# Kernel tuning notes

Hardware: AMD Instinct MI355X
Metric: run time of the kernel (lower is better)

Reference implementation:

```python
import jax, jax.numpy as jnp
import numpy as np

DS = 16
NUM_INPUTS = 13
WIDTH = 64
DEPTH = 5
NUM_OUTPUTS = 3
# channels of the per-pixel MLP: input gets 4*log2(ds) cosine coord channels
CH = [NUM_INPUTS + 4 * int(np.log2(DS))] + [WIDTH] * (DEPTH - 1) + [NUM_OUTPUTS]


def _splits():
    biases, weights, idx = [], [], 0
    for l in range(len(CH) - 1):
        nci, nco = CH[l], CH[l + 1]
        biases.append((idx, idx + nco)); idx += nco
        weights.append((idx, idx + nco * nci)); idx += nco * nci
    return biases, weights, idx

BIAS_SPLITS, WEIGHT_SPLITS, NUM_PARAMS = _splits()


def _get_coords(bs, h, w, ds):
    """Cosine positional encoding, 4 channels per octave of ds."""
    two_pi = 2.0 * np.pi
    chans = []
    f = ds
    x = jnp.arange(w, dtype=jnp.float32)
    y = jnp.arange(h, dtype=jnp.float32)
    while f > 1:
        px = two_pi * jnp.remainder(x, f) / f  # [w]
        py = two_pi * jnp.remainder(y, f) / f  # [h]
        xcos = jnp.broadcast_to(jnp.cos(px)[None, None, None, :], (bs, 1, h, w))
        xsin = jnp.broadcast_to(jnp.sin(px)[None, None, None, :], (bs, 1, h, w))
        ycos = jnp.broadcast_to(jnp.cos(py)[None, None, :, None], (bs, 1, h, w))
        ysin = jnp.broadcast_to(jnp.sin(py)[None, None, :, None], (bs, 1, h, w))
        chans += [xcos, xsin, ycos, ysin]
        f //= 2
    return jnp.concatenate(chans, axis=1)  # [bs, 4*log2(ds), h, w]


def setup_inputs() -> dict:
    key = jax.random.key(0)
    k1, k2 = jax.random.split(key)
    bs, h, w = 4, 512, 512
    h_lr, w_lr = h // DS, w // DS
    highres = jax.random.normal(k1, (bs, NUM_INPUTS, h, w), dtype=jnp.float32)
    lr_params = jax.random.normal(k2, (bs, NUM_PARAMS, h_lr, w_lr), dtype=jnp.float32)
    return {"highres": highres, "lr_params": lr_params}


def reference(highres, lr_params):
    k = DS
    bs, _, h, w = highres.shape
    _, _, h_lr, w_lr = lr_params.shape

    coords = _get_coords(bs, h, w, k)
    x = jnp.concatenate([highres, coords], axis=1)  # [bs, nci0, h, w]
    nci0 = x.shape[1]

    # unfold into k*k tiles per low-res pixel: [bs, h_lr, w_lr, k*k, nci0]
    tiles = (x.reshape(bs, nci0, h_lr, k, w_lr, k)
              .transpose(0, 2, 4, 3, 5, 1)
              .reshape(bs, h_lr, w_lr, k * k, nci0))

    out = tiles
    n_layers = len(CH) - 1
    for l in range(n_layers):
        nci, nco = CH[l], CH[l + 1]
        ws, we = WEIGHT_SPLITS[l]
        b0, b1 = BIAS_SPLITS[l]
        w_ = (lr_params[:, ws:we].transpose(0, 2, 3, 1)
              .reshape(bs, h_lr, w_lr, nci, nco))
        b_ = (lr_params[:, b0:b1].transpose(0, 2, 3, 1)
              .reshape(bs, h_lr, w_lr, 1, nco))
        out = jnp.einsum('bhwpi,bhwio->bhwpo', out, w_) + b_
        if l < n_layers - 1:
            out = jnp.where(out >= 0, out, 0.01 * out)  # leaky_relu(0.01)
        else:
            out = jnp.tanh(out)

    # fold tiles back to [bs, num_outputs, h, w]
    out = (out.reshape(bs, h_lr, w_lr, k, k, NUM_OUTPUTS)
            .transpose(0, 5, 1, 3, 2, 4)
            .reshape(bs, NUM_OUTPUTS, h, w))
    return out
```

## Files before the change

### kernel.cpp

```cpp
#include <hip/hip_runtime.h>
#include <math.h>

#define NCH   14595
#define WROW  14596
#define HR_C  13
#define IMG_H 512
#define IMG_W 512
#define BS    4


__global__ __launch_bounds__(256) void transpose_params(const float* __restrict__ lp,
                                                        float* __restrict__ wsT) {
    __shared__ float tile[64][65];
    int bid = blockIdx.x;
    int pt = bid & 15;
    int t  = bid >> 4;
    int ct = t % 229;
    int b  = t / 229;
    int c0 = ct * 64, p0 = pt * 64;
    int tp = threadIdx.x & 63;
    int tr = threadIdx.x >> 6;
#pragma unroll
    for (int s = 0; s < 16; s++) {
        int c = c0 + tr + s * 4;
        if (c < NCH)
            tile[tr + s * 4][tp] = lp[((size_t)b * NCH + c) * 1024 + p0 + tp];
    }
    __syncthreads();
#pragma unroll
    for (int s = 0; s < 16; s++) {
        int p = p0 + tr + s * 4;
        int c = c0 + tp;
        if (c < NCH)
            wsT[((size_t)b * 1024 + p) * WROW + c] = tile[tp][tr + s * 4];
    }
}

__device__ __forceinline__ void block_sync_lds() {
    __builtin_amdgcn_sched_barrier(0);
    asm volatile("s_waitcnt lgkmcnt(0)" ::: "memory");
    __builtin_amdgcn_s_barrier();
    __builtin_amdgcn_sched_barrier(0);
}

template<int NCI>
__device__ __forceinline__ void mlp_layer(const float* __restrict__ actT,
                                          const float* __restrict__ wbuf,
                                          int px0, int o0, float acc[4][8]) {
#pragma unroll
    for (int j = 0; j < 8; j++) {
        float bv = wbuf[o0 + j];
        acc[0][j] = bv; acc[1][j] = bv; acc[2][j] = bv; acc[3][j] = bv;
    }
#pragma unroll 4
    for (int k = 0; k < NCI; k++) {
        float4 a  = *(const float4*)&actT[k * 128 + px0];
        float4 w0 = *(const float4*)&wbuf[64 + (k << 6) + o0];
        float4 w1 = *(const float4*)&wbuf[64 + (k << 6) + o0 + 4];
        float av[4] = {a.x, a.y, a.z, a.w};
        float wv[8] = {w0.x, w0.y, w0.z, w0.w, w1.x, w1.y, w1.z, w1.w};
#pragma unroll
        for (int i = 0; i < 4; i++)
#pragma unroll
            for (int j = 0; j < 8; j++)
                acc[i][j] = fmaf(av[i], wv[j], acc[i][j]);
    }
}

__global__ __launch_bounds__(256, 3) void asap_main(const float* __restrict__ hr,
                                                    const float* __restrict__ lp,
                                                    const float* __restrict__ wsT,
                                                    float* __restrict__ out,
                                                    int use_ws) {
    __shared__ __align__(16) float actT[64 * 128];
    __shared__ __align__(16) float wbuf[4160];

    int bid0 = blockIdx.x;
    int bid  = ((bid0 & 7) << 10) | (bid0 >> 3);

    int half = bid & 1;
    int x    = (bid >> 1) & 31;
    int y    = (bid >> 6) & 31;
    int b    = bid >> 11;
    int tid  = threadIdx.x;
    int pix  = y * 32 + x;

    const size_t wrow_base = ((size_t)b * 1024 + pix) * WROW;
    const float* lp_base   = lp + (size_t)b * NCH * 1024 + pix;

    float4 rv[5];
    float  rt0 = 0.f;
    auto stage_load = [&](int off, int len) {
        int n4 = len >> 2;
        if (use_ws) {
            const float4* s4 = (const float4*)(wsT + wrow_base + off);
#pragma unroll
            for (int i = 0; i < 5; i++) {
                int j = tid + (i << 8);
                if (j < n4) rv[i] = s4[j];
            }
            if (tid < (len & 3)) rt0 = wsT[wrow_base + off + (len & ~3) + tid];
        } else {
#pragma unroll
            for (int i = 0; i < 5; i++) {
                int j = tid + (i << 8);
                if (j < n4) {
                    int e = off + (j << 2);
                    rv[i].x = lp_base[(size_t)(e + 0) << 10];
                    rv[i].y = lp_base[(size_t)(e + 1) << 10];
                    rv[i].z = lp_base[(size_t)(e + 2) << 10];
                    rv[i].w = lp_base[(size_t)(e + 3) << 10];
                }
            }
            if (tid < (len & 3)) rt0 = lp_base[(size_t)(off + (len & ~3) + tid) << 10];
        }
    };
    auto stage_store = [&](int len) {
        int n4 = len >> 2;
        float4* d4 = (float4*)wbuf;
#pragma unroll
        for (int i = 0; i < 5; i++) {
            int j = tid + (i << 8);
            if (j < n4) d4[j] = rv[i];
        }
        if (tid < (len & 3)) wbuf[(len & ~3) + tid] = rt0;
    };

    {
        if (use_ws) {
            const float4* s4 = (const float4*)(wsT + wrow_base);
            float4* d4 = (float4*)wbuf;
            for (int j = tid; j < 480; j += 256) d4[j] = s4[j];
        } else {
            for (int j = tid; j < 1920; j += 256) wbuf[j] = lp_base[(size_t)j << 10];
        }
        int Y0 = y * 16 + half * 8, X0 = x * 16;
        for (int t = tid; t < HR_C * 128; t += 256) {
            int c = t >> 7, p = t & 127;
            int row = p >> 4, kx = p & 15;
            actT[c * 128 + p] =
                hr[(((size_t)b * HR_C + c) * IMG_H + Y0 + row) * IMG_W + X0 + kx];
        }
        if (tid < 128) {
            int p = tid, row = p >> 4, kx = p & 15;
            int kyg = half * 8 + row;
            const float two_pi = 6.28318530717958647692f;
            int f = 16;
#pragma unroll
            for (int fi = 0; fi < 4; fi++) {
                float ax = two_pi * (float)(kx & (f - 1)) / (float)f;
                float ay = two_pi * (float)(kyg & (f - 1)) / (float)f;
                actT[(13 + 4 * fi + 0) * 128 + p] = cosf(ax);
                actT[(13 + 4 * fi + 1) * 128 + p] = sinf(ax);
                actT[(13 + 4 * fi + 2) * 128 + p] = cosf(ay);
                actT[(13 + 4 * fi + 3) * 128 + p] = sinf(ay);
                f >>= 1;
            }
        }
    }
    block_sync_lds();

    int pg = tid & 31, og = tid >> 5;
    int px0 = pg << 2, o0 = og << 3;
    float acc[4][8];

    auto writeback = [&]() {
#pragma unroll
        for (int j = 0; j < 8; j++) {
            float4 v;
            v.x = acc[0][j]; v.y = acc[1][j]; v.z = acc[2][j]; v.w = acc[3][j];
            v.x = v.x >= 0.f ? v.x : 0.01f * v.x;
            v.y = v.y >= 0.f ? v.y : 0.01f * v.y;
            v.z = v.z >= 0.f ? v.z : 0.01f * v.z;
            v.w = v.w >= 0.f ? v.w : 0.01f * v.w;
            *(float4*)&actT[(o0 + j) * 128 + px0] = v;
        }
    };

    stage_load(1920, 4160);
    mlp_layer<29>(actT, wbuf, px0, o0, acc);
    block_sync_lds();
    writeback();
    stage_store(4160);
    block_sync_lds();

    stage_load(6080, 4160);
    mlp_layer<64>(actT, wbuf, px0, o0, acc);
    block_sync_lds();
    writeback();
    stage_store(4160);
    block_sync_lds();

    stage_load(10240, 4160);
    mlp_layer<64>(actT, wbuf, px0, o0, acc);
    block_sync_lds();
    writeback();
    stage_store(4160);
    block_sync_lds();

    stage_load(14400, 195);
    mlp_layer<64>(actT, wbuf, px0, o0, acc);
    block_sync_lds();
    writeback();
    stage_store(195);
    block_sync_lds();

    if (tid < 128) {
        int p = tid;
        float s0 = wbuf[0], s1 = wbuf[1], s2 = wbuf[2];
#pragma unroll 4
        for (int k = 0; k < 64; k++) {
            float a = actT[k * 128 + p];
            s0 = fmaf(a, wbuf[3 + k * 3 + 0], s0);
            s1 = fmaf(a, wbuf[3 + k * 3 + 1], s1);
            s2 = fmaf(a, wbuf[3 + k * 3 + 2], s2);
        }
        int row = p >> 4, kx = p & 15;
        int Y = y * 16 + half * 8 + row, X = x * 16 + kx;
        size_t base = ((size_t)b * 3) * IMG_H * IMG_W + (size_t)Y * IMG_W + X;
        out[base]                             = tanhf(s0);
        out[base + (size_t)IMG_H * IMG_W]     = tanhf(s1);
        out[base + (size_t)2 * IMG_H * IMG_W] = tanhf(s2);
    }
}

extern "C" void kernel_launch(void* const* d_in, const int* in_sizes, int n_in,
                              void* d_out, int out_size, void* d_ws, size_t ws_size,
                              hipStream_t stream) {
    const float* hr = (const float*)d_in[0];
    const float* lp = (const float*)d_in[1];
    float* out = (float*)d_out;
    float* wsT = (float*)d_ws;

    size_t need = (size_t)BS * 1024 * WROW * sizeof(float);
    int use_ws = (ws_size >= need) ? 1 : 0;

    if (use_ws) {
        transpose_params<<<BS * 229 * 16, 256, 0, stream>>>(lp, wsT);
    }
    asap_main<<<8192, 256, 0, stream>>>(hr, lp, wsT, out, use_ws);
}
```

Measured before the change: 533.9 us.

## Read per-pixel weights directly from global memory instead of staging in LDS

Removes the LDS weight buffer and its register-staged prefetch, so each thread reads its weight float4s and biases straight from the transposed workspace row, which goes through the cache since all threads in a block share one row. Freeing LDS lets the launch bound rise to four blocks per SIMD group, and the use_ws branch becomes a template parameter. Leaky-relu becomes fmaxf. The cost is that weight loads now hit global memory or cache latency inside the FMA inner loop instead of LDS, and the overlap of the next layer's weight prefetch with compute is lost.

```diff
diff --git a/kernel.cpp b/kernel.cpp
--- a/kernel.cpp
+++ b/kernel.cpp
@@ -43,37 +43,63 @@
     __builtin_amdgcn_sched_barrier(0);
 }
 
-template<int NCI>
+template<int NCI, bool USE_WS>
 __device__ __forceinline__ void mlp_layer(const float* __restrict__ actT,
-                                          const float* __restrict__ wbuf,
+                                          const float* __restrict__ wrow,
+                                          const float* __restrict__ lp_col,
+                                          int loff,
                                           int px0, int o0, float acc[4][8]) {
-#pragma unroll
-    for (int j = 0; j < 8; j++) {
-        float bv = wbuf[o0 + j];
-        acc[0][j] = bv; acc[1][j] = bv; acc[2][j] = bv; acc[3][j] = bv;
+    if (USE_WS) {
+        float4 b0 = *(const float4*)&wrow[o0];
+        float4 b1 = *(const float4*)&wrow[o0 + 4];
+#pragma unroll
+        for (int i = 0; i < 4; i++) {
+            acc[i][0] = b0.x; acc[i][1] = b0.y; acc[i][2] = b0.z; acc[i][3] = b0.w;
+            acc[i][4] = b1.x; acc[i][5] = b1.y; acc[i][6] = b1.z; acc[i][7] = b1.w;
+        }
+    } else {
+#pragma unroll
+        for (int j = 0; j < 8; j++) {
+            float bv = lp_col[(size_t)(loff + o0 + j) << 10];
+#pragma unroll
+            for (int i = 0; i < 4; i++) acc[i][j] = bv;
+        }
     }
 #pragma unroll 4
     for (int k = 0; k < NCI; k++) {
-        float4 a  = *(const float4*)&actT[k * 128 + px0];
-        float4 w0 = *(const float4*)&wbuf[64 + (k << 6) + o0];
-        float4 w1 = *(const float4*)&wbuf[64 + (k << 6) + o0 + 4];
-        float av[4] = {a.x, a.y, a.z, a.w};
-        float wv[8] = {w0.x, w0.y, w0.z, w0.w, w1.x, w1.y, w1.z, w1.w};
-#pragma unroll
-        for (int i = 0; i < 4; i++)
-#pragma unroll
-            for (int j = 0; j < 8; j++)
-                acc[i][j] = fmaf(av[i], wv[j], acc[i][j]);
-    }
-}
-
-__global__ __launch_bounds__(256, 3) void asap_main(const float* __restrict__ hr,
+        float4 a = *(const float4*)&actT[k * 128 + px0];
+        float4 w0, w1;
+        if (USE_WS) {
+            w0 = *(const float4*)&wrow[64 + (k << 6) + o0];
+            w1 = *(const float4*)&wrow[64 + (k << 6) + o0 + 4];
+        } else {
+            int e = loff + 64 + (k << 6) + o0;
+            w0.x = lp_col[(size_t)(e + 0) << 10]; w0.y = lp_col[(size_t)(e + 1) << 10];
+            w0.z = lp_col[(size_t)(e + 2) << 10]; w0.w = lp_col[(size_t)(e + 3) << 10];
+            w1.x = lp_col[(size_t)(e + 4) << 10]; w1.y = lp_col[(size_t)(e + 5) << 10];
+            w1.z = lp_col[(size_t)(e + 6) << 10]; w1.w = lp_col[(size_t)(e + 7) << 10];
+        }
+#pragma unroll
+        for (int i = 0; i < 4; i++) {
+            float av = (i == 0) ? a.x : (i == 1) ? a.y : (i == 2) ? a.z : a.w;
+            acc[i][0] = fmaf(av, w0.x, acc[i][0]);
+            acc[i][1] = fmaf(av, w0.y, acc[i][1]);
+            acc[i][2] = fmaf(av, w0.z, acc[i][2]);
+            acc[i][3] = fmaf(av, w0.w, acc[i][3]);
+            acc[i][4] = fmaf(av, w1.x, acc[i][4]);
+            acc[i][5] = fmaf(av, w1.y, acc[i][5]);
+            acc[i][6] = fmaf(av, w1.z, acc[i][6]);
+            acc[i][7] = fmaf(av, w1.w, acc[i][7]);
+        }
+    }
+}
+
+template<bool USE_WS>
+__global__ __launch_bounds__(256, 4) void asap_main(const float* __restrict__ hr,
                                                     const float* __restrict__ lp,
                                                     const float* __restrict__ wsT,
-                                                    float* __restrict__ out,
-                                                    int use_ws) {
+                                                    float* __restrict__ out) {
     __shared__ __align__(16) float actT[64 * 128];
-    __shared__ __align__(16) float wbuf[4160];
 
     int bid0 = blockIdx.x;
     int bid  = ((bid0 & 7) << 10) | (bid0 >> 3);
@@ -85,55 +111,10 @@
     int tid  = threadIdx.x;
     int pix  = y * 32 + x;
 
-    const size_t wrow_base = ((size_t)b * 1024 + pix) * WROW;
-    const float* lp_base   = lp + (size_t)b * NCH * 1024 + pix;
-
-    float4 rv[5];
-    float  rt0 = 0.f;
-    auto stage_load = [&](int off, int len) {
-        int n4 = len >> 2;
-        if (use_ws) {
-            const float4* s4 = (const float4*)(wsT + wrow_base + off);
-#pragma unroll
-            for (int i = 0; i < 5; i++) {
-                int j = tid + (i << 8);
-                if (j < n4) rv[i] = s4[j];
-            }
-            if (tid < (len & 3)) rt0 = wsT[wrow_base + off + (len & ~3) + tid];
-        } else {
-#pragma unroll
-            for (int i = 0; i < 5; i++) {
-                int j = tid + (i << 8);
-                if (j < n4) {
-                    int e = off + (j << 2);
-                    rv[i].x = lp_base[(size_t)(e + 0) << 10];
-                    rv[i].y = lp_base[(size_t)(e + 1) << 10];
-                    rv[i].z = lp_base[(size_t)(e + 2) << 10];
-                    rv[i].w = lp_base[(size_t)(e + 3) << 10];
-                }
-            }
-            if (tid < (len & 3)) rt0 = lp_base[(size_t)(off + (len & ~3) + tid) << 10];
-        }
-    };
-    auto stage_store = [&](int len) {
-        int n4 = len >> 2;
-        float4* d4 = (float4*)wbuf;
-#pragma unroll
-        for (int i = 0; i < 5; i++) {
-            int j = tid + (i << 8);
-            if (j < n4) d4[j] = rv[i];
-        }
-        if (tid < (len & 3)) wbuf[(len & ~3) + tid] = rt0;
-    };
+    const float* wrow   = wsT + ((size_t)b * 1024 + pix) * WROW;
+    const float* lp_col = lp + (size_t)b * NCH * 1024 + pix;
 
     {
-        if (use_ws) {
-            const float4* s4 = (const float4*)(wsT + wrow_base);
-            float4* d4 = (float4*)wbuf;
-            for (int j = tid; j < 480; j += 256) d4[j] = s4[j];
-        } else {
-            for (int j = tid; j < 1920; j += 256) wbuf[j] = lp_base[(size_t)j << 10];
-        }
         int Y0 = y * 16 + half * 8, X0 = x * 16;
         for (int t = tid; t < HR_C * 128; t += 256) {
             int c = t >> 7, p = t & 127;
@@ -169,51 +150,60 @@
         for (int j = 0; j < 8; j++) {
             float4 v;
             v.x = acc[0][j]; v.y = acc[1][j]; v.z = acc[2][j]; v.w = acc[3][j];
-            v.x = v.x >= 0.f ? v.x : 0.01f * v.x;
-            v.y = v.y >= 0.f ? v.y : 0.01f * v.y;
-            v.z = v.z >= 0.f ? v.z : 0.01f * v.z;
-            v.w = v.w >= 0.f ? v.w : 0.01f * v.w;
+            v.x = fmaxf(v.x, 0.01f * v.x);
+            v.y = fmaxf(v.y, 0.01f * v.y);
+            v.z = fmaxf(v.z, 0.01f * v.z);
+            v.w = fmaxf(v.w, 0.01f * v.w);
             *(float4*)&actT[(o0 + j) * 128 + px0] = v;
         }
     };
 
-    stage_load(1920, 4160);
-    mlp_layer<29>(actT, wbuf, px0, o0, acc);
-    block_sync_lds();
-    writeback();
-    stage_store(4160);
-    block_sync_lds();
-
-    stage_load(6080, 4160);
-    mlp_layer<64>(actT, wbuf, px0, o0, acc);
-    block_sync_lds();
-    writeback();
-    stage_store(4160);
-    block_sync_lds();
-
-    stage_load(10240, 4160);
-    mlp_layer<64>(actT, wbuf, px0, o0, acc);
-    block_sync_lds();
-    writeback();
-    stage_store(4160);
-    block_sync_lds();
-
-    stage_load(14400, 195);
-    mlp_layer<64>(actT, wbuf, px0, o0, acc);
-    block_sync_lds();
-    writeback();
-    stage_store(195);
+    mlp_layer<29, USE_WS>(actT, wrow + 0,     lp_col, 0,     px0, o0, acc);
+    block_sync_lds();
+    writeback();
+    block_sync_lds();
+
+    mlp_layer<64, USE_WS>(actT, wrow + 1920,  lp_col, 1920,  px0, o0, acc);
+    block_sync_lds();
+    writeback();
+    block_sync_lds();
+
+    mlp_layer<64, USE_WS>(actT, wrow + 6080,  lp_col, 6080,  px0, o0, acc);
+    block_sync_lds();
+    writeback();
+    block_sync_lds();
+
+    mlp_layer<64, USE_WS>(actT, wrow + 10240, lp_col, 10240, px0, o0, acc);
+    block_sync_lds();
+    writeback();
     block_sync_lds();
 
     if (tid < 128) {
         int p = tid;
-        float s0 = wbuf[0], s1 = wbuf[1], s2 = wbuf[2];
+        float s0, s1, s2;
+        if (USE_WS) {
+            s0 = wrow[14400]; s1 = wrow[14401]; s2 = wrow[14402];
+        } else {
+            s0 = lp_col[(size_t)14400 << 10];
+            s1 = lp_col[(size_t)14401 << 10];
+            s2 = lp_col[(size_t)14402 << 10];
+        }
 #pragma unroll 4
         for (int k = 0; k < 64; k++) {
             float a = actT[k * 128 + p];
-            s0 = fmaf(a, wbuf[3 + k * 3 + 0], s0);
-            s1 = fmaf(a, wbuf[3 + k * 3 + 1], s1);
-            s2 = fmaf(a, wbuf[3 + k * 3 + 2], s2);
+            float w0, w1, w2;
+            if (USE_WS) {
+                w0 = wrow[14403 + k * 3 + 0];
+                w1 = wrow[14403 + k * 3 + 1];
+                w2 = wrow[14403 + k * 3 + 2];
+            } else {
+                w0 = lp_col[(size_t)(14403 + k * 3 + 0) << 10];
+                w1 = lp_col[(size_t)(14403 + k * 3 + 1) << 10];
+                w2 = lp_col[(size_t)(14403 + k * 3 + 2) << 10];
+            }
+            s0 = fmaf(a, w0, s0);
+            s1 = fmaf(a, w1, s1);
+            s2 = fmaf(a, w2, s2);
         }
         int row = p >> 4, kx = p & 15;
         int Y = y * 16 + half * 8 + row, X = x * 16 + kx;
@@ -233,10 +223,10 @@
     float* wsT = (float*)d_ws;
 
     size_t need = (size_t)BS * 1024 * WROW * sizeof(float);
-    int use_ws = (ws_size >= need) ? 1 : 0;
-
-    if (use_ws) {
+    if (ws_size >= need) {
         transpose_params<<<BS * 229 * 16, 256, 0, stream>>>(lp, wsT);
-    }
-    asap_main<<<8192, 256, 0, stream>>>(hr, lp, wsT, out, use_ws);
-}
+        asap_main<true><<<8192, 256, 0, stream>>>(hr, lp, wsT, out);
+    } else {
+        asap_main<false><<<8192, 256, 0, stream>>>(hr, lp, wsT, out);
+    }
+}
```

Result: slower. 637.3 us (+19.4%).
